# Performance work log

Measured on AMD Instinct MI355X. Metric: run time of the kernel, lower is better.

The kernel has to match this reference:

```python
import jax, jax.numpy as jnp
import numpy as np

B, N, C = 2, 10000, 128
NH, NP = 4, 20          # n_heads, n_points (n_levels = 1)
DH = C // NH            # head dim = 32
HW = 100                # spatial shape (100, 100), N = HW*HW


def setup_inputs() -> dict:
    key = jax.random.key(0)
    ks = jax.random.split(key, 12)
    s = 0.05  # small param scale so softmax/linears stay well-conditioned
    return {
        "query": jax.random.normal(ks[0], (B, N, C), jnp.float32),
        "query_pos": jax.random.normal(ks[1], (B, N, C), jnp.float32),
        "W_val": jax.random.normal(ks[2], (C, C), jnp.float32) * s,
        "b_val": jax.random.normal(ks[3], (C,), jnp.float32) * s,
        "W_off": jax.random.normal(ks[4], (NH * NP * 2, C), jnp.float32) * s,
        "b_off": jax.random.normal(ks[5], (NH * NP * 2,), jnp.float32) * s,
        "W_attn": jax.random.normal(ks[6], (NH * NP, C), jnp.float32) * s,
        "b_attn": jax.random.normal(ks[7], (NH * NP,), jnp.float32) * s,
        "W_out1": jax.random.normal(ks[8], (C, C), jnp.float32) * s,
        "b_out1": jax.random.normal(ks[9], (C,), jnp.float32) * s,
        "W_out2": jax.random.normal(ks[10], (C, C), jnp.float32) * s,
        "b_out2": jax.random.normal(ks[11], (C,), jnp.float32) * s,
    }


def _msdeform_forward(query, query_pos, W_val, b_val, W_off, b_off,
                      W_attn, b_attn, W_out1, b_out1, W_out2, b_out2):
    residual = query
    q = query + query_pos  # pos added; value branch also uses q (query.clone())

    # reference points: meshgrid of (z, x) normalized to (0,1), shape (N, 2)
    lin = (jnp.arange(HW, dtype=jnp.float32) + 0.5) / HW
    ref_z, ref_x = jnp.meshgrid(lin, lin, indexing="ij")
    ref = jnp.stack([ref_z.reshape(-1), ref_x.reshape(-1)], axis=-1)  # (N,2)

    # projections
    value = (q @ W_val.T + b_val).reshape(B, N, NH, DH).transpose(0, 2, 1, 3)  # (B,NH,N,DH)
    off = (q @ W_off.T + b_off).reshape(B, N, NH, NP, 2)
    attn = jax.nn.softmax((q @ W_attn.T + b_attn).reshape(B, N, NH, NP), axis=-1)

    # sampling locations in normalized coords; offset normalizer = (W, H) = (100, 100)
    loc = ref[None, :, None, None, :] + off / HW  # (B,N,NH,NP,2)

    # grid_sample bilinear, align_corners=False, zeros padding:
    # pixel coord = loc * size - 0.5
    x = (loc[..., 0] * HW - 0.5).transpose(0, 2, 1, 3)  # (B,NH,N,NP)
    y = (loc[..., 1] * HW - 0.5).transpose(0, 2, 1, 3)
    aw = attn.transpose(0, 2, 1, 3)                     # (B,NH,N,NP)

    x0f = jnp.floor(x); y0f = jnp.floor(y)
    wx1 = x - x0f; wy1 = y - y0f
    wx0 = 1.0 - wx1; wy0 = 1.0 - wy1
    ix0 = x0f.astype(jnp.int32); iy0 = y0f.astype(jnp.int32)
    ix1 = ix0 + 1; iy1 = iy0 + 1

    def gather(ix, iy):
        valid = ((ix >= 0) & (ix < HW) & (iy >= 0) & (iy < HW)).astype(value.dtype)
        idx = jnp.clip(iy, 0, HW - 1) * HW + jnp.clip(ix, 0, HW - 1)  # (B,NH,N,NP)
        g = jnp.take_along_axis(value, idx.reshape(B, NH, N * NP, 1), axis=2)
        return g.reshape(B, NH, N, NP, DH) * valid[..., None]

    sampled = ((wx0 * wy0)[..., None] * gather(ix0, iy0)
               + (wx1 * wy0)[..., None] * gather(ix1, iy0)
               + (wx0 * wy1)[..., None] * gather(ix0, iy1)
               + (wx1 * wy1)[..., None] * gather(ix1, iy1))  # (B,NH,N,NP,DH)

    out = (sampled * aw[..., None]).sum(axis=3)             # (B,NH,N,DH)
    out = out.transpose(0, 2, 1, 3).reshape(B, N, C)
    out = out @ W_out1.T + b_out1   # MSDeformAttn.output_proj
    out = out @ W_out2.T + b_out2   # wrapper output_proj
    return out + residual           # dropout is identity in eval


def reference(query, query_pos, W_val, b_val, W_off, b_off,
              W_attn, b_attn, W_out1, b_out1, W_out2, b_out2):
    return _msdeform_forward(query, query_pos, W_val, b_val, W_off, b_off,
                             W_attn, b_attn, W_out1, b_out1, W_out2, b_out2)
```

## Files before the change

### kernel.cpp

```cpp
#include <hip/hip_runtime.h>
#include <hip/hip_bf16.h>
#include <math.h>

#define NTOK 10000
#define BATCH 2
#define CDIM 128
#define NHEAD 4
#define NPNT 20
#define DHEAD 32
#define HWDIM 100
#define MROWS (BATCH * NTOK)
#define OCAT 368
#define OPAD 384
#define PTOK 8
#define PHALO 4
#define PDIM 16
#define NPATCH 13
#define CELLPAD 40

typedef __attribute__((ext_vector_type(8))) short short8v;
typedef __attribute__((ext_vector_type(4))) short short4v;
typedef __attribute__((ext_vector_type(4))) float f32x4;

__device__ __forceinline__ float bfbits(short s) {
  union { unsigned u; float f; } c;
  c.u = ((unsigned)(unsigned short)s) << 16;
  return c.f;
}

__global__ __launch_bounds__(128) void fold_kernel(
    const float* __restrict__ W1, const float* __restrict__ b1,
    const float* __restrict__ W2, const float* __restrict__ b2,
    float* __restrict__ Wc, float* __restrict__ bc) {
  __shared__ float w2row[128];
  __shared__ float red[128];
  int o = blockIdx.x, c = threadIdx.x;
  w2row[c] = W2[o * 128 + c];
  __syncthreads();
  float acc = 0.f;
  for (int k = 0; k < 128; ++k) acc += w2row[k] * W1[k * 128 + c];
  Wc[o * 128 + c] = acc;
  red[c] = w2row[c] * b1[c];
  __syncthreads();
  for (int s = 64; s > 0; s >>= 1) {
    if (c < s) red[c] += red[c + s];
    __syncthreads();
  }
  if (c == 0) bc[o] = b2[o] + red[0];
}

__global__ __launch_bounds__(128) void conv_kernel(
    const float* __restrict__ W_val, const float* __restrict__ b_val,
    const float* __restrict__ W_off, const float* __restrict__ b_off,
    const float* __restrict__ W_attn, const float* __restrict__ b_attn,
    const float* __restrict__ Wc, __hip_bfloat16* __restrict__ Wcat,
    float* __restrict__ bcat, __hip_bfloat16* __restrict__ Wc_bf) {
  int r = blockIdx.x, c = threadIdx.x;
  if (r < OPAD) {
    float v = 0.f, bv = 0.f;
    if (r < 128) { v = W_val[r * 128 + c]; bv = b_val[r]; }
    else if (r < 288) { v = W_off[(r - 128) * 128 + c]; bv = b_off[r - 128]; }
    else if (r < OCAT) { v = W_attn[(r - 288) * 128 + c]; bv = b_attn[r - 288]; }
    Wcat[(size_t)r * 128 + c] = __float2bfloat16(v);
    if (c == 0) bcat[r] = bv;
  } else {
    int rr = r - OPAD;
    Wc_bf[(size_t)rr * 128 + c] = __float2bfloat16(Wc[rr * 128 + c]);
  }
}

template <int MODE, int AKIND>
__global__ __launch_bounds__(256) void mfma_proj_kernel(
    const float* __restrict__ src_f, const float* __restrict__ src2,
    const __hip_bfloat16* __restrict__ src_b,
    const __hip_bfloat16* __restrict__ Wb, const float* __restrict__ bias,
    __hip_bfloat16* __restrict__ value, float* __restrict__ offo,
    float* __restrict__ attno, float* __restrict__ out,
    const float* __restrict__ resid, int M, int Otiles, int Ototal) {
  __shared__ __hip_bfloat16 qa[64][128];
  __shared__ __hip_bfloat16 wb[64][128];
  const int t = threadIdx.x;
  const int r0 = blockIdx.x * 64;

#pragma unroll
  for (int i = 0; i < 4; ++i) {
    int lin = t + 256 * i;
    int r = lin >> 4;
    int g = lin & 15;
    if (AKIND == 0) {
      int c = g << 3;
      float4 v0 = make_float4(0.f, 0.f, 0.f, 0.f);
      float4 v1 = make_float4(0.f, 0.f, 0.f, 0.f);
      if (r0 + r < M) {
        const float* p = src_f + (size_t)(r0 + r) * CDIM + c;
        v0 = *(const float4*)p;
        v1 = *(const float4*)(p + 4);
        const float* p2 = src2 + (size_t)(r0 + r) * CDIM + c;
        float4 u0 = *(const float4*)p2;
        float4 u1 = *(const float4*)(p2 + 4);
        v0.x += u0.x; v0.y += u0.y; v0.z += u0.z; v0.w += u0.w;
        v1.x += u1.x; v1.y += u1.y; v1.z += u1.z; v1.w += u1.w;
      }
      __hip_bfloat16* dst = &qa[r][(g ^ (r & 7)) << 3];
      dst[0] = __float2bfloat16(v0.x); dst[1] = __float2bfloat16(v0.y);
      dst[2] = __float2bfloat16(v0.z); dst[3] = __float2bfloat16(v0.w);
      dst[4] = __float2bfloat16(v1.x); dst[5] = __float2bfloat16(v1.y);
      dst[6] = __float2bfloat16(v1.z); dst[7] = __float2bfloat16(v1.w);
    } else {
      short8v v = (short8v)(short)0;
      if (r0 + r < M)
        v = *(const short8v*)(src_b + (size_t)(r0 + r) * CDIM + (g << 3));
      *(short8v*)&qa[r][(g ^ (r & 7)) << 3] = v;
    }
  }
  __syncthreads();

  const int wid = t >> 6;
  const int lane = t & 63;
  const int wr = (wid >> 1) * 32;
  const int wc = (wid & 1) * 32;
  const int lrow = lane & 15;
  const int lk = lane >> 4;

  short8v afr[4][2];
  {
    int ra0 = wr + lrow, ra1 = wr + 16 + lrow;
#pragma unroll
    for (int kk = 0; kk < 4; ++kk) {
      int gb = kk * 4 + lk;
      afr[kk][0] = *(const short8v*)&qa[ra0][(gb ^ (ra0 & 7)) << 3];
      afr[kk][1] = *(const short8v*)&qa[ra1][(gb ^ (ra1 & 7)) << 3];
    }
  }

  for (int ti = 0; ti < Otiles; ++ti) {
    const int ot = (blockIdx.y * Otiles + ti) * 64;
    __syncthreads();
#pragma unroll
    for (int i = 0; i < 4; ++i) {
      int lin = t + 256 * i;
      int r = lin >> 4;
      int g = lin & 15;
      short8v w = *(const short8v*)(Wb + (size_t)(ot + r) * 128 + (g << 3));
      *(short8v*)&wb[r][(g ^ (r & 7)) << 3] = w;
    }
    __syncthreads();

    f32x4 acc[2][2];
#pragma unroll
    for (int mi = 0; mi < 2; ++mi)
#pragma unroll
      for (int ni = 0; ni < 2; ++ni) acc[mi][ni] = (f32x4)(0.f);

#pragma unroll
    for (int kk = 0; kk < 4; ++kk) {
      const int gb = kk * 4 + lk;
      int rb0 = wc + lrow, rb1 = wc + 16 + lrow;
      short8v b0 = *(const short8v*)&wb[rb0][(gb ^ (rb0 & 7)) << 3];
      short8v b1 = *(const short8v*)&wb[rb1][(gb ^ (rb1 & 7)) << 3];
      acc[0][0] = __builtin_amdgcn_mfma_f32_16x16x32_bf16(afr[kk][0], b0, acc[0][0], 0, 0, 0);
      acc[0][1] = __builtin_amdgcn_mfma_f32_16x16x32_bf16(afr[kk][0], b1, acc[0][1], 0, 0, 0);
      acc[1][0] = __builtin_amdgcn_mfma_f32_16x16x32_bf16(afr[kk][1], b0, acc[1][0], 0, 0, 0);
      acc[1][1] = __builtin_amdgcn_mfma_f32_16x16x32_bf16(afr[kk][1], b1, acc[1][1], 0, 0, 0);
    }

#pragma unroll
    for (int mi = 0; mi < 2; ++mi) {
#pragma unroll
      for (int ni = 0; ni < 2; ++ni) {
#pragma unroll
        for (int reg = 0; reg < 4; ++reg) {
          int r = r0 + wr + mi * 16 + (lane >> 4) * 4 + reg;
          int o = ot + wc + ni * 16 + (lane & 15);
          if (r >= M || o >= Ototal) continue;
          float v = acc[mi][ni][reg] + bias[o];
          if (MODE == 1) {
            out[(size_t)r * CDIM + o] = v + resid[(size_t)r * CDIM + o];
          } else {
            int b = r >= NTOK ? 1 : 0;
            int n = r - b * NTOK;
            if (o < 128) {
              int h = o >> 5, rem = o & 31;
              value[(((size_t)b * NHEAD + h) * NTOK + n) * 32 + rem] =
                  __float2bfloat16(v);
            } else if (o < 288) {
              int oo = o - 128, h = oo / 40, rem = oo - h * 40;
              offo[(((size_t)b * NHEAD + h) * NTOK + n) * 40 + rem] = v;
            } else {
              int oo = o - 288, h = oo / 20, rem = oo - h * 20;
              attno[(((size_t)b * NHEAD + h) * NTOK + n) * 20 + rem] = v;
            }
          }
        }
      }
    }
  }
}

__global__ __launch_bounds__(256) void sample_kernel(
    const __hip_bfloat16* __restrict__ value, const float* __restrict__ off,
    const float* __restrict__ attn, __hip_bfloat16* __restrict__ outat) {
  const int s = blockIdx.x & 7;
  const int pidx = blockIdx.x >> 3;
  const int PI = pidx % NPATCH, PJ = pidx / NPATCH;
  const int I0 = PI * PTOK, J0 = PJ * PTOK;
  const int b = s >> 2, h = s & 3;

  __shared__ __hip_bfloat16 patch[PDIM * PDIM][CELLPAD];
  const __hip_bfloat16* vglob = value + (size_t)s * NTOK * DHEAD;

#pragma unroll
  for (int it = 0; it < 4; ++it) {
    int lin = threadIdx.x + 256 * it;
    int cell = lin >> 2, part = lin & 3;
    int py = cell >> 4, px = cell & 15;
    int gy = J0 - PHALO + py;
    int gx = I0 - PHALO + px;
    short8v v = (short8v)(short)0;
    if (gy >= 0 && gy < HWDIM && gx >= 0 && gx < HWDIM)
      v = *(const short8v*)(vglob + ((size_t)(gy * HWDIM + gx)) * DHEAD +
                            part * 8);
    *(short8v*)&patch[cell][part * 8] = v;
  }
  __syncthreads();

  const int d4 = threadIdx.x & 7;
  const int slot = threadIdx.x >> 3;

  for (int tt = 0; tt < 2; ++tt) {
    const int tok = slot + 32 * tt;
    const int li = tok & 7, lj = tok >> 3;
    const int i = I0 + li, j = J0 + lj;
    if (i >= HWDIM || j >= HWDIM) continue;
    const int n = i * HWDIM + j;

    union { float4 v4[10]; float f[40]; } of;
    union { float4 v4[5]; float f[20]; } at;
    {
      const float4* o4 = (const float4*)(off + ((size_t)s * NTOK + n) * 40);
      const float4* a4 = (const float4*)(attn + ((size_t)s * NTOK + n) * 20);
#pragma unroll
      for (int q = 0; q < 10; ++q) of.v4[q] = o4[q];
#pragma unroll
      for (int q = 0; q < 5; ++q) at.v4[q] = a4[q];
    }

    float ssum = 0.f;
#pragma unroll
    for (int p = 0; p < NPNT; ++p) {
      at.f[p] = __expf(at.f[p]);
      ssum += at.f[p];
    }
    const float inv = 1.f / ssum;

    const float fi = (float)i, fj = (float)j;
    float ax = 0.f, ay = 0.f, az = 0.f, aw4 = 0.f;
#pragma unroll
    for (int p = 0; p < NPNT; ++p) {
      float x = fi + of.f[2 * p];
      float y = fj + of.f[2 * p + 1];
      float aw = at.f[p] * inv;
      float x0f = floorf(x), y0f = floorf(y);
      int ix0 = (int)x0f, iy0 = (int)y0f;
      float wx1 = x - x0f, wy1 = y - y0f;
      float wx0 = 1.f - wx1, wy0 = 1.f - wy1;
      float w00 = aw * wy0 * wx0, w01 = aw * wy0 * wx1;
      float w10 = aw * wy1 * wx0, w11 = aw * wy1 * wx1;
      int ly = iy0 - (J0 - PHALO);
      int lx = ix0 - (I0 - PHALO);
      if (ly >= 0 && ly <= PDIM - 2 && lx >= 0 && lx <= PDIM - 2) {
        const __hip_bfloat16* pb = &patch[ly * PDIM + lx][d4 * 4];
        short4v g00 = *(const short4v*)pb;
        short4v g01 = *(const short4v*)(pb + CELLPAD);
        short4v g10 = *(const short4v*)(pb + PDIM * CELLPAD);
        short4v g11 = *(const short4v*)(pb + PDIM * CELLPAD + CELLPAD);
        ax += w00 * bfbits(g00.x) + w01 * bfbits(g01.x) + w10 * bfbits(g10.x) + w11 * bfbits(g11.x);
        ay += w00 * bfbits(g00.y) + w01 * bfbits(g01.y) + w10 * bfbits(g10.y) + w11 * bfbits(g11.y);
        az += w00 * bfbits(g00.z) + w01 * bfbits(g01.z) + w10 * bfbits(g10.z) + w11 * bfbits(g11.z);
        aw4 += w00 * bfbits(g00.w) + w01 * bfbits(g01.w) + w10 * bfbits(g10.w) + w11 * bfbits(g11.w);
      } else {
        float wgt[4] = {w00, w01, w10, w11};
#pragma unroll
        for (int cy = 0; cy < 2; ++cy) {
          int iy = iy0 + cy;
          if (iy < 0 || iy >= HWDIM) continue;
#pragma unroll
          for (int cx = 0; cx < 2; ++cx) {
            int ix = ix0 + cx;
            if (ix < 0 || ix >= HWDIM) continue;
            float w = wgt[cy * 2 + cx];
            short4v g = *(const short4v*)(vglob +
                                          ((size_t)(iy * HWDIM + ix)) * DHEAD +
                                          d4 * 4);
            ax += w * bfbits(g.x); ay += w * bfbits(g.y);
            az += w * bfbits(g.z); aw4 += w * bfbits(g.w);
          }
        }
      }
    }
    union { short4v v4; __hip_bfloat16 hh[4]; } o;
    o.hh[0] = __float2bfloat16(ax); o.hh[1] = __float2bfloat16(ay);
    o.hh[2] = __float2bfloat16(az); o.hh[3] = __float2bfloat16(aw4);
    *(short4v*)(outat + ((size_t)b * NTOK + n) * CDIM + h * DHEAD + d4 * 4) =
        o.v4;
  }
}

extern "C" void kernel_launch(void* const* d_in, const int* in_sizes, int n_in,
                              void* d_out, int out_size, void* d_ws,
                              size_t ws_size, hipStream_t stream) {
  const float* query = (const float*)d_in[0];
  const float* query_pos = (const float*)d_in[1];
  const float* W_val = (const float*)d_in[2];
  const float* b_val = (const float*)d_in[3];
  const float* W_off = (const float*)d_in[4];
  const float* b_off = (const float*)d_in[5];
  const float* W_attn = (const float*)d_in[6];
  const float* b_attn = (const float*)d_in[7];
  const float* W_out1 = (const float*)d_in[8];
  const float* b_out1 = (const float*)d_in[9];
  const float* W_out2 = (const float*)d_in[10];
  const float* b_out2 = (const float*)d_in[11];
  float* out = (float*)d_out;

  char* ws = (char*)d_ws;
  __hip_bfloat16* value = (__hip_bfloat16*)ws;
  ws += (size_t)MROWS * CDIM * 2;
  float* offb = (float*)ws;
  ws += (size_t)MROWS * 160 * 4;
  float* attnb = (float*)ws;
  ws += (size_t)MROWS * 80 * 4;
  __hip_bfloat16* outat = (__hip_bfloat16*)ws;
  ws += (size_t)MROWS * CDIM * 2;
  float* Wc = (float*)ws; ws += 128 * 128 * 4;
  float* bc = (float*)ws; ws += 128 * 4;
  float* bcat = (float*)ws; ws += OPAD * 4;
  __hip_bfloat16* Wcat = (__hip_bfloat16*)ws; ws += (size_t)OPAD * 128 * 2;
  __hip_bfloat16* Wc_bf = (__hip_bfloat16*)ws;

  fold_kernel<<<128, 128, 0, stream>>>(W_out1, b_out1, W_out2, b_out2, Wc, bc);
  conv_kernel<<<OPAD + 128, 128, 0, stream>>>(W_val, b_val, W_off, b_off,
                                              W_attn, b_attn, Wc, Wcat, bcat,
                                              Wc_bf);

  mfma_proj_kernel<0, 0><<<dim3(313, 2), 256, 0, stream>>>(
      query, query_pos, nullptr, Wcat, bcat, value, offb, attnb, nullptr,
      nullptr, MROWS, 3, OCAT);

  sample_kernel<<<8 * NPATCH * NPATCH, 256, 0, stream>>>(value, offb, attnb,
                                                         outat);

  mfma_proj_kernel<1, 1><<<dim3(313, 2), 256, 0, stream>>>(
      nullptr, nullptr, outat, Wc_bf, bc, nullptr, nullptr, nullptr, out,
      query, MROWS, 1, 128);
}
```

Baseline: 66.13 us.

## Merge weight prep kernels and widen sampling to 8 channels per thread

Fuses the weight-folding and bf16 conversion kernels into one prep kernel, dropping a launch and the fp32 intermediate buffer. The sampling kernel now maps 4 threads per token with 8 channels each, using 16-byte LDS/global loads and vector accumulators. The softmax normalisation is moved out of the point loop to a single multiply at the end. This trades more registers per thread and half the threads-per-token parallelism for fewer, wider memory ops. The bank-conflict pattern may also change.

Result: faster. 60.82 us (-8.0%).

```diff
diff --git a/kernel.cpp b/kernel.cpp
--- a/kernel.cpp
+++ b/kernel.cpp
@@ -22,50 +22,54 @@
 typedef __attribute__((ext_vector_type(4))) short short4v;
 typedef __attribute__((ext_vector_type(4))) float f32x4;
 
-__device__ __forceinline__ float bfbits(short s) {
-  union { unsigned u; float f; } c;
-  c.u = ((unsigned)(unsigned short)s) << 16;
-  return c.f;
-}
-
-__global__ __launch_bounds__(128) void fold_kernel(
-    const float* __restrict__ W1, const float* __restrict__ b1,
-    const float* __restrict__ W2, const float* __restrict__ b2,
-    float* __restrict__ Wc, float* __restrict__ bc) {
-  __shared__ float w2row[128];
-  __shared__ float red[128];
-  int o = blockIdx.x, c = threadIdx.x;
-  w2row[c] = W2[o * 128 + c];
-  __syncthreads();
-  float acc = 0.f;
-  for (int k = 0; k < 128; ++k) acc += w2row[k] * W1[k * 128 + c];
-  Wc[o * 128 + c] = acc;
-  red[c] = w2row[c] * b1[c];
-  __syncthreads();
-  for (int s = 64; s > 0; s >>= 1) {
-    if (c < s) red[c] += red[c + s];
-    __syncthreads();
-  }
-  if (c == 0) bc[o] = b2[o] + red[0];
-}
-
-__global__ __launch_bounds__(128) void conv_kernel(
+__device__ __forceinline__ float asf(unsigned u) {
+  union { unsigned u; float f; } c; c.u = u; return c.f;
+}
+
+__device__ __forceinline__ void acc_cell(const __hip_bfloat16* p, float w,
+                                         f32x4& a0, f32x4& a1) {
+  int4 u = *(const int4*)p;
+  f32x4 g0, g1;
+  g0.x = asf(((unsigned)u.x) << 16); g0.y = asf(((unsigned)u.x) & 0xFFFF0000u);
+  g0.z = asf(((unsigned)u.y) << 16); g0.w = asf(((unsigned)u.y) & 0xFFFF0000u);
+  g1.x = asf(((unsigned)u.z) << 16); g1.y = asf(((unsigned)u.z) & 0xFFFF0000u);
+  g1.z = asf(((unsigned)u.w) << 16); g1.w = asf(((unsigned)u.w) & 0xFFFF0000u);
+  a0 += g0 * w;
+  a1 += g1 * w;
+}
+
+__global__ __launch_bounds__(128) void prep_kernel(
     const float* __restrict__ W_val, const float* __restrict__ b_val,
     const float* __restrict__ W_off, const float* __restrict__ b_off,
     const float* __restrict__ W_attn, const float* __restrict__ b_attn,
-    const float* __restrict__ Wc, __hip_bfloat16* __restrict__ Wcat,
-    float* __restrict__ bcat, __hip_bfloat16* __restrict__ Wc_bf) {
-  int r = blockIdx.x, c = threadIdx.x;
-  if (r < OPAD) {
+    const float* __restrict__ W1, const float* __restrict__ b1,
+    const float* __restrict__ W2, const float* __restrict__ b2,
+    __hip_bfloat16* __restrict__ Wcat, float* __restrict__ bcat,
+    __hip_bfloat16* __restrict__ Wc_bf, float* __restrict__ bc) {
+  __shared__ float w2row[128];
+  __shared__ float red[128];
+  const int blk = blockIdx.x, c = threadIdx.x;
+  if (blk < OPAD) {
     float v = 0.f, bv = 0.f;
-    if (r < 128) { v = W_val[r * 128 + c]; bv = b_val[r]; }
-    else if (r < 288) { v = W_off[(r - 128) * 128 + c]; bv = b_off[r - 128]; }
-    else if (r < OCAT) { v = W_attn[(r - 288) * 128 + c]; bv = b_attn[r - 288]; }
-    Wcat[(size_t)r * 128 + c] = __float2bfloat16(v);
-    if (c == 0) bcat[r] = bv;
+    if (blk < 128) { v = W_val[blk * 128 + c]; bv = b_val[blk]; }
+    else if (blk < 288) { v = W_off[(blk - 128) * 128 + c]; bv = b_off[blk - 128]; }
+    else if (blk < OCAT) { v = W_attn[(blk - 288) * 128 + c]; bv = b_attn[blk - 288]; }
+    Wcat[(size_t)blk * 128 + c] = __float2bfloat16(v);
+    if (c == 0) bcat[blk] = bv;
   } else {
-    int rr = r - OPAD;
-    Wc_bf[(size_t)rr * 128 + c] = __float2bfloat16(Wc[rr * 128 + c]);
+    const int o = blk - OPAD;
+    w2row[c] = W2[o * 128 + c];
+    __syncthreads();
+    float acc = 0.f;
+    for (int k = 0; k < 128; ++k) acc += w2row[k] * W1[k * 128 + c];
+    Wc_bf[(size_t)o * 128 + c] = __float2bfloat16(acc);
+    red[c] = w2row[c] * b1[c];
+    __syncthreads();
+    for (int s = 64; s > 0; s >>= 1) {
+      if (c < s) red[c] += red[c + s];
+      __syncthreads();
+    }
+    if (c == 0) bc[o] = b2[o] + red[0];
   }
 }
 
@@ -224,86 +228,79 @@
   }
   __syncthreads();
 
-  const int d4 = threadIdx.x & 7;
-  const int slot = threadIdx.x >> 3;
-
-  for (int tt = 0; tt < 2; ++tt) {
-    const int tok = slot + 32 * tt;
-    const int li = tok & 7, lj = tok >> 3;
-    const int i = I0 + li, j = J0 + lj;
-    if (i >= HWDIM || j >= HWDIM) continue;
-    const int n = i * HWDIM + j;
-
-    union { float4 v4[10]; float f[40]; } of;
-    union { float4 v4[5]; float f[20]; } at;
-    {
-      const float4* o4 = (const float4*)(off + ((size_t)s * NTOK + n) * 40);
-      const float4* a4 = (const float4*)(attn + ((size_t)s * NTOK + n) * 20);
-#pragma unroll
-      for (int q = 0; q < 10; ++q) of.v4[q] = o4[q];
-#pragma unroll
-      for (int q = 0; q < 5; ++q) at.v4[q] = a4[q];
-    }
-
-    float ssum = 0.f;
-#pragma unroll
-    for (int p = 0; p < NPNT; ++p) {
-      at.f[p] = __expf(at.f[p]);
-      ssum += at.f[p];
-    }
-    const float inv = 1.f / ssum;
-
-    const float fi = (float)i, fj = (float)j;
-    float ax = 0.f, ay = 0.f, az = 0.f, aw4 = 0.f;
-#pragma unroll
-    for (int p = 0; p < NPNT; ++p) {
-      float x = fi + of.f[2 * p];
-      float y = fj + of.f[2 * p + 1];
-      float aw = at.f[p] * inv;
-      float x0f = floorf(x), y0f = floorf(y);
-      int ix0 = (int)x0f, iy0 = (int)y0f;
-      float wx1 = x - x0f, wy1 = y - y0f;
-      float wx0 = 1.f - wx1, wy0 = 1.f - wy1;
-      float w00 = aw * wy0 * wx0, w01 = aw * wy0 * wx1;
-      float w10 = aw * wy1 * wx0, w11 = aw * wy1 * wx1;
-      int ly = iy0 - (J0 - PHALO);
-      int lx = ix0 - (I0 - PHALO);
-      if (ly >= 0 && ly <= PDIM - 2 && lx >= 0 && lx <= PDIM - 2) {
-        const __hip_bfloat16* pb = &patch[ly * PDIM + lx][d4 * 4];
-        short4v g00 = *(const short4v*)pb;
-        short4v g01 = *(const short4v*)(pb + CELLPAD);
-        short4v g10 = *(const short4v*)(pb + PDIM * CELLPAD);
-        short4v g11 = *(const short4v*)(pb + PDIM * CELLPAD + CELLPAD);
-        ax += w00 * bfbits(g00.x) + w01 * bfbits(g01.x) + w10 * bfbits(g10.x) + w11 * bfbits(g11.x);
-        ay += w00 * bfbits(g00.y) + w01 * bfbits(g01.y) + w10 * bfbits(g10.y) + w11 * bfbits(g11.y);
-        az += w00 * bfbits(g00.z) + w01 * bfbits(g01.z) + w10 * bfbits(g10.z) + w11 * bfbits(g11.z);
-        aw4 += w00 * bfbits(g00.w) + w01 * bfbits(g01.w) + w10 * bfbits(g10.w) + w11 * bfbits(g11.w);
-      } else {
-        float wgt[4] = {w00, w01, w10, w11};
-#pragma unroll
-        for (int cy = 0; cy < 2; ++cy) {
-          int iy = iy0 + cy;
-          if (iy < 0 || iy >= HWDIM) continue;
-#pragma unroll
-          for (int cx = 0; cx < 2; ++cx) {
-            int ix = ix0 + cx;
-            if (ix < 0 || ix >= HWDIM) continue;
-            float w = wgt[cy * 2 + cx];
-            short4v g = *(const short4v*)(vglob +
-                                          ((size_t)(iy * HWDIM + ix)) * DHEAD +
-                                          d4 * 4);
-            ax += w * bfbits(g.x); ay += w * bfbits(g.y);
-            az += w * bfbits(g.z); aw4 += w * bfbits(g.w);
-          }
+  const int dl = threadIdx.x & 3;
+  const int tok = threadIdx.x >> 2;
+  const int li = tok & 7, lj = tok >> 3;
+  const int i = I0 + li, j = J0 + lj;
+  if (i >= HWDIM || j >= HWDIM) return;
+  const int n = i * HWDIM + j;
+
+  union { float4 v4[10]; float f[40]; } of;
+  union { float4 v4[5]; float f[20]; } at;
+  {
+    const float4* o4 = (const float4*)(off + ((size_t)s * NTOK + n) * 40);
+    const float4* a4 = (const float4*)(attn + ((size_t)s * NTOK + n) * 20);
+#pragma unroll
+    for (int q = 0; q < 10; ++q) of.v4[q] = o4[q];
+#pragma unroll
+    for (int q = 0; q < 5; ++q) at.v4[q] = a4[q];
+  }
+
+  float ssum = 0.f;
+#pragma unroll
+  for (int p = 0; p < NPNT; ++p) {
+    at.f[p] = __expf(at.f[p]);
+    ssum += at.f[p];
+  }
+  const float inv = 1.f / ssum;
+
+  const float fi = (float)i, fj = (float)j;
+  f32x4 a0 = (f32x4)(0.f), a1 = (f32x4)(0.f);
+#pragma unroll
+  for (int p = 0; p < NPNT; ++p) {
+    float x = fi + of.f[2 * p];
+    float y = fj + of.f[2 * p + 1];
+    float aw = at.f[p];
+    float x0f = floorf(x), y0f = floorf(y);
+    int ix0 = (int)x0f, iy0 = (int)y0f;
+    float wx1 = x - x0f, wy1 = y - y0f;
+    float wx0 = 1.f - wx1, wy0 = 1.f - wy1;
+    float wya = aw * wy0, wyb = aw * wy1;
+    float w00 = wya * wx0, w01 = wya * wx1;
+    float w10 = wyb * wx0, w11 = wyb * wx1;
+    int ly = iy0 - (J0 - PHALO);
+    int lx = ix0 - (I0 - PHALO);
+    if (ly >= 0 && ly <= PDIM - 2 && lx >= 0 && lx <= PDIM - 2) {
+      const __hip_bfloat16* pb = &patch[ly * PDIM + lx][dl * 8];
+      acc_cell(pb, w00, a0, a1);
+      acc_cell(pb + CELLPAD, w01, a0, a1);
+      acc_cell(pb + PDIM * CELLPAD, w10, a0, a1);
+      acc_cell(pb + PDIM * CELLPAD + CELLPAD, w11, a0, a1);
+    } else {
+      float wgt[4] = {w00, w01, w10, w11};
+#pragma unroll
+      for (int cy = 0; cy < 2; ++cy) {
+        int iy = iy0 + cy;
+        if (iy < 0 || iy >= HWDIM) continue;
+#pragma unroll
+        for (int cx = 0; cx < 2; ++cx) {
+          int ix = ix0 + cx;
+          if (ix < 0 || ix >= HWDIM) continue;
+          acc_cell(vglob + ((size_t)(iy * HWDIM + ix)) * DHEAD + dl * 8,
+                   wgt[cy * 2 + cx], a0, a1);
         }
       }
     }
-    union { short4v v4; __hip_bfloat16 hh[4]; } o;
-    o.hh[0] = __float2bfloat16(ax); o.hh[1] = __float2bfloat16(ay);
-    o.hh[2] = __float2bfloat16(az); o.hh[3] = __float2bfloat16(aw4);
-    *(short4v*)(outat + ((size_t)b * NTOK + n) * CDIM + h * DHEAD + d4 * 4) =
-        o.v4;
-  }
+  }
+
+  union { short8v v8; __hip_bfloat16 hh[8]; } o;
+#pragma unroll
+  for (int k = 0; k < 4; ++k) {
+    o.hh[k] = __float2bfloat16(a0[k] * inv);
+    o.hh[4 + k] = __float2bfloat16(a1[k] * inv);
+  }
+  *(short8v*)(outat + ((size_t)b * NTOK + n) * CDIM + h * DHEAD + dl * 8) =
+      o.v8;
 }
 
 extern "C" void kernel_launch(void* const* d_in, const int* in_sizes, int n_in,
@@ -332,16 +329,14 @@
   ws += (size_t)MROWS * 80 * 4;
   __hip_bfloat16* outat = (__hip_bfloat16*)ws;
   ws += (size_t)MROWS * CDIM * 2;
-  float* Wc = (float*)ws; ws += 128 * 128 * 4;
   float* bc = (float*)ws; ws += 128 * 4;
   float* bcat = (float*)ws; ws += OPAD * 4;
   __hip_bfloat16* Wcat = (__hip_bfloat16*)ws; ws += (size_t)OPAD * 128 * 2;
   __hip_bfloat16* Wc_bf = (__hip_bfloat16*)ws;
 
-  fold_kernel<<<128, 128, 0, stream>>>(W_out1, b_out1, W_out2, b_out2, Wc, bc);
-  conv_kernel<<<OPAD + 128, 128, 0, stream>>>(W_val, b_val, W_off, b_off,
-                                              W_attn, b_attn, Wc, Wcat, bcat,
-                                              Wc_bf);
+  prep_kernel<<<OPAD + 128, 128, 0, stream>>>(
+      W_val, b_val, W_off, b_off, W_attn, b_attn, W_out1, b_out1, W_out2,
+      b_out2, Wcat, bcat, Wc_bf, bc);
 
   mfma_proj_kernel<0, 0><<<dim3(313, 2), 256, 0, stream>>>(
       query, query_pos, nullptr, Wcat, bcat, value, offb, attnb, nullptr,
```
